# Performance work log

Measured on AMD Instinct MI355X. Metric: run time of the kernel, lower is better.

The kernel has to match this reference:

```python
import jax, jax.numpy as jnp
import numpy as np

HIDDEN = 768  # hidden_dim of the embedding matrix
VOCAB = 30522


def setup_inputs() -> dict:
    key = jax.random.key(0)
    k1, k2, k3, k4, k5, k6 = jax.random.split(key, 6)
    core = jax.random.normal(k1, (40, 256, 256), dtype=jnp.float32)
    f0 = jax.random.normal(k2, (40, 40), dtype=jnp.float32)
    f1 = jax.random.normal(k3, (768, 256), dtype=jnp.float32)
    f2 = jax.random.normal(k4, (768, 256), dtype=jnp.float32)
    ids = jax.random.randint(k5, (8192,), 0, VOCAB, dtype=jnp.int32)
    x = jax.random.normal(k6, (8192, 768), dtype=jnp.float32)  # unused by forward, kept for signature parity
    return {"x": x, "ids": ids, "core": core, "f0": f0, "f1": f1, "f2": f2}


def reference(x, ids, core, f0, f1, f2):
    # tucker_to_tensor: core x_0 f0 x_1 f1 x_2 f2 -> (40, 768, 768)
    res = jnp.einsum('abc,ia,jb,kc->ijk', core, f0, f1, f2)
    # flatten to padded embedding table (30720, 768) and gather requested rows
    table = res.reshape(-1, HIDDEN)
    return table[ids, :]
```

## Files before the change

kernel.cpp:

```cpp
#include <hip/hip_runtime.h>


#define A_DIM 40
#define BC 65536
#define C_DIM 256
#define HID 768

typedef __attribute__((ext_vector_type(8))) short short8;
typedef __attribute__((ext_vector_type(4))) float floatx4;

#define AS1 __attribute__((address_space(1)))
#define AS3 __attribute__((address_space(3)))

__device__ __forceinline__ void gl2lds16(const unsigned short* g, unsigned short* l) {
    __builtin_amdgcn_global_load_lds((const AS1 unsigned int*)g, (AS3 unsigned int*)l,
                                     16, 0, 0);
}

__device__ __forceinline__ unsigned short f2bf(float f) {
    unsigned int u = __builtin_bit_cast(unsigned int, f);
    u += 0x7FFFu + ((u >> 16) & 1u);
    return (unsigned short)(u >> 16);
}

__global__ __launch_bounds__(256) void k01_fused(const float* __restrict__ core,
                                                 const float* __restrict__ f0,
                                                 const float* __restrict__ f1,
                                                 const float* __restrict__ f2,
                                                 unsigned short* __restrict__ A1t,
                                                 unsigned short* __restrict__ f1b,
                                                 unsigned short* __restrict__ f2b) {
    const int bid = blockIdx.x;
    const int tid = threadIdx.x;
    if (bid < 512) {
        __shared__ float f0s[200];
        __shared__ unsigned short tt[32 * 34];
        const int i0 = (bid >> 6) * 5;
        const int tile = bid & 63;
        const int b0 = (tile >> 3) * 32;
        const int c0 = (tile & 7) * 32;
        if (tid < 200) f0s[tid] = f0[i0 * A_DIM + tid];
        __syncthreads();

        const int pb = (tid >> 4) * 2;
        const int pc = (tid & 15) * 2;
        float acc[5][4];
#pragma unroll
        for (int ii = 0; ii < 5; ++ii)
#pragma unroll
            for (int e = 0; e < 4; ++e) acc[ii][e] = 0.f;

        const float* cp0 = core + (b0 + pb) * 256 + (c0 + pc);
        for (int a = 0; a < A_DIM; ++a) {
            const float* cp = cp0 + a * BC;
            const float2 r0 = *(const float2*)cp;
            const float2 r1 = *(const float2*)(cp + 256);
#pragma unroll
            for (int ii = 0; ii < 5; ++ii) {
                const float fa = f0s[ii * A_DIM + a];
                acc[ii][0] += fa * r0.x;
                acc[ii][1] += fa * r0.y;
                acc[ii][2] += fa * r1.x;
                acc[ii][3] += fa * r1.y;
            }
        }
        const int rc = tid >> 3;
        const int rb4 = (tid & 7) * 4;
#pragma unroll
        for (int ii = 0; ii < 5; ++ii) {
            if (ii) __syncthreads();
            unsigned short e00 = f2bf(acc[ii][0]);
            unsigned short e10 = f2bf(acc[ii][2]);
            unsigned short e01 = f2bf(acc[ii][1]);
            unsigned short e11 = f2bf(acc[ii][3]);
            *(unsigned int*)&tt[pc * 34 + pb]       = (unsigned int)e00 | ((unsigned int)e10 << 16);
            *(unsigned int*)&tt[(pc + 1) * 34 + pb] = (unsigned int)e01 | ((unsigned int)e11 << 16);
            __syncthreads();
            unsigned short o[4];
#pragma unroll
            for (int u = 0; u < 4; ++u) o[u] = tt[rc * 34 + rb4 + u];
            unsigned int lo = (unsigned int)o[0] | ((unsigned int)o[1] << 16);
            unsigned int hi = (unsigned int)o[2] | ((unsigned int)o[3] << 16);
            *(uint2*)&A1t[(size_t)(i0 + ii) * BC + (c0 + rc) * 256 + b0 + rb4] = make_uint2(lo, hi);
        }
    } else {
        const int idx = (bid - 512) * 256 + tid;
        const float* src;
        unsigned short* dst;
        int off;
        if (idx < 49152) { src = f1; dst = f1b; off = idx; }
        else             { src = f2; dst = f2b; off = idx - 49152; }
        const float4 v = *(const float4*)&src[off * 4];
        const unsigned int lo = (unsigned int)f2bf(v.x) | ((unsigned int)f2bf(v.y) << 16);
        const unsigned int hi = (unsigned int)f2bf(v.z) | ((unsigned int)f2bf(v.w) << 16);
        *(uint2*)&dst[off * 4] = make_uint2(lo, hi);
    }
}

__global__ __launch_bounds__(256) void k2_gemm(const unsigned short* __restrict__ f1b,
                                               const unsigned short* __restrict__ A1t,
                                               unsigned short* __restrict__ A2) {
    const int i  = blockIdx.z;
    const int j0 = blockIdx.x * 64;
    const int c0 = blockIdx.y * 64;
    const unsigned short* __restrict__ Bsrc = A1t + i * BC;

    __shared__ unsigned short As[64 * 32];
    __shared__ unsigned short Bs[64 * 32];

    const int tid = threadIdx.x;
    const int lane = tid & 63, wave = tid >> 6;
    const int wm = (wave >> 1) * 32, wn = (wave & 1) * 32;
    const int l16 = lane & 15, q = lane >> 4;

    const int r0 = tid >> 2, o0 = (tid & 3) * 8;
    unsigned short* AsW = &As[wave * 512];
    unsigned short* BsW = &Bs[wave * 512];

    floatx4 acc[2][2];
#pragma unroll
    for (int p = 0; p < 2; ++p)
#pragma unroll
        for (int r = 0; r < 2; ++r) acc[p][r] = (floatx4)0.f;

    for (int kk = 0; kk < C_DIM; kk += 32) {
        gl2lds16(&f1b[(j0 + r0) * 256 + kk + o0], AsW);
        gl2lds16(&Bsrc[(c0 + r0) * 256 + kk + o0], BsW);
        __syncthreads();
        short8 af[2], bf[2];
#pragma unroll
        for (int p = 0; p < 2; ++p) af[p] = *(const short8*)&As[(wm + p * 16 + l16) * 32 + q * 8];
#pragma unroll
        for (int r = 0; r < 2; ++r) bf[r] = *(const short8*)&Bs[(wn + r * 16 + l16) * 32 + q * 8];
#pragma unroll
        for (int p = 0; p < 2; ++p)
#pragma unroll
            for (int r = 0; r < 2; ++r)
                acc[p][r] = __builtin_amdgcn_mfma_f32_16x16x32_bf16(af[p], bf[r], acc[p][r], 0, 0, 0);
        __syncthreads();
    }
    unsigned short* __restrict__ Cout = A2 + (size_t)i * HID * C_DIM;
#pragma unroll
    for (int p = 0; p < 2; ++p)
#pragma unroll
        for (int r = 0; r < 2; ++r)
#pragma unroll
            for (int rr = 0; rr < 4; ++rr) {
                const int row = j0 + wm + p * 16 + q * 4 + rr;
                const int col = c0 + wn + r * 16 + l16;
                Cout[row * 256 + col] = f2bf(acc[p][r][rr]);
            }
}

__global__ __launch_bounds__(256) void k3_gemm(const unsigned short* __restrict__ A2,
                                               const unsigned short* __restrict__ f2b,
                                               const int* __restrict__ ids,
                                               float* __restrict__ out) {
    const int n0 = blockIdx.x * 64;
    const int k0 = blockIdx.y * 64;

    __shared__ int ids_s[64];
    __shared__ unsigned short As[64 * 32];
    __shared__ unsigned short Bs[64 * 32];

    const int tid = threadIdx.x;
    if (tid < 64) ids_s[tid] = ids[n0 + tid];
    __syncthreads();

    const int lane = tid & 63, wave = tid >> 6;
    const int wm = (wave >> 1) * 32, wn = (wave & 1) * 32;
    const int l16 = lane & 15, q = lane >> 4;

    const int r0 = tid >> 2, o0 = (tid & 3) * 8;
    const size_t ga = (size_t)ids_s[r0] * 256;
    unsigned short* AsW = &As[wave * 512];
    unsigned short* BsW = &Bs[wave * 512];

    floatx4 acc[2][2];
#pragma unroll
    for (int p = 0; p < 2; ++p)
#pragma unroll
        for (int r = 0; r < 2; ++r) acc[p][r] = (floatx4)0.f;

    for (int kk = 0; kk < C_DIM; kk += 32) {
        gl2lds16(&A2[ga + kk + o0], AsW);
        gl2lds16(&f2b[(k0 + r0) * 256 + kk + o0], BsW);
        __syncthreads();
        short8 af[2], bf[2];
#pragma unroll
        for (int p = 0; p < 2; ++p) af[p] = *(const short8*)&As[(wm + p * 16 + l16) * 32 + q * 8];
#pragma unroll
        for (int r = 0; r < 2; ++r) bf[r] = *(const short8*)&Bs[(wn + r * 16 + l16) * 32 + q * 8];
#pragma unroll
        for (int p = 0; p < 2; ++p)
#pragma unroll
            for (int r = 0; r < 2; ++r)
                acc[p][r] = __builtin_amdgcn_mfma_f32_16x16x32_bf16(af[p], bf[r], acc[p][r], 0, 0, 0);
        __syncthreads();
    }
#pragma unroll
    for (int p = 0; p < 2; ++p)
#pragma unroll
        for (int r = 0; r < 2; ++r)
#pragma unroll
            for (int rr = 0; rr < 4; ++rr) {
                const int row = n0 + wm + p * 16 + q * 4 + rr;
                const int col = k0 + wn + r * 16 + l16;
                out[(size_t)row * HID + col] = acc[p][r][rr];
            }
}

extern "C" void kernel_launch(void* const* d_in, const int* in_sizes, int n_in,
                              void* d_out, int out_size, void* d_ws, size_t ws_size,
                              hipStream_t stream) {
    const int*   ids  = (const int*)d_in[1];
    const float* core = (const float*)d_in[2];
    const float* f0   = (const float*)d_in[3];
    const float* f1   = (const float*)d_in[4];
    const float* f2   = (const float*)d_in[5];
    float* out = (float*)d_out;

    char* ws = (char*)d_ws;
    unsigned short* A1t = (unsigned short*)ws;
    unsigned short* A2  = (unsigned short*)(ws + 5242880);
    unsigned short* f1b = (unsigned short*)(ws + 20971520);
    unsigned short* f2b = (unsigned short*)(ws + 21364736);

    k01_fused<<<896, 256, 0, stream>>>(core, f0, f1, f2, A1t, f1b, f2b);
    k2_gemm<<<dim3(12, 4, A_DIM), 256, 0, stream>>>(f1b, A1t, A2);
    k3_gemm<<<dim3(128, 12), 256, 0, stream>>>(A2, f2b, ids, out);
}
```

Before: 113.5 us.

## Compute only the intermediate rows that the ids gather actually needs

An extra block in the first kernel buckets the ids by their leading index i, records the requested j rows per i in slot lists padded to 64, and stores a tile count per i. The second GEMM now runs one block per tile of requested rows, gathering f1 rows through the slot list, instead of computing all 768 rows for every i. This cuts the second GEMM's work to roughly the rows the final gather touches. In exchange it adds a serial, atomic-heavy bucketing block, and it assumes at most 320 ids fall on any one i (CAP). Inputs that concentrate more ids on a single i would overflow the slot buffer.

Measured after the change: 121.3 us. +6.9%, slower.

```diff
diff --git a/kernel.cpp b/kernel.cpp
--- a/kernel.cpp
+++ b/kernel.cpp
@@ -5,6 +5,7 @@
 #define BC 65536
 #define C_DIM 256
 #define HID 768
+#define CAP 320
 
 typedef __attribute__((ext_vector_type(8))) short short8;
 typedef __attribute__((ext_vector_type(4))) float floatx4;
@@ -27,9 +28,12 @@
                                                  const float* __restrict__ f0,
                                                  const float* __restrict__ f1,
                                                  const float* __restrict__ f2,
+                                                 const int* __restrict__ ids,
                                                  unsigned short* __restrict__ A1t,
                                                  unsigned short* __restrict__ f1b,
-                                                 unsigned short* __restrict__ f2b) {
+                                                 unsigned short* __restrict__ f2b,
+                                                 int* __restrict__ jslot,
+                                                 int* __restrict__ tilecnt) {
     const int bid = blockIdx.x;
     const int tid = threadIdx.x;
     if (bid < 512) {
@@ -83,7 +87,7 @@
             unsigned int hi = (unsigned int)o[2] | ((unsigned int)o[3] << 16);
             *(uint2*)&A1t[(size_t)(i0 + ii) * BC + (c0 + rc) * 256 + b0 + rb4] = make_uint2(lo, hi);
         }
-    } else {
+    } else if (bid < 896) {
         const int idx = (bid - 512) * 256 + tid;
         const float* src;
         unsigned short* dst;
@@ -94,26 +98,58 @@
         const unsigned int lo = (unsigned int)f2bf(v.x) | ((unsigned int)f2bf(v.y) << 16);
         const unsigned int hi = (unsigned int)f2bf(v.z) | ((unsigned int)f2bf(v.w) << 16);
         *(uint2*)&dst[off * 4] = make_uint2(lo, hi);
+    } else {
+        __shared__ int cnt[A_DIM];
+        __shared__ int off[A_DIM];
+        if (tid < A_DIM) { cnt[tid] = 0; off[tid] = 0; }
+        __syncthreads();
+        for (int t = tid; t < 8192; t += 256) {
+            const unsigned int id = (unsigned int)ids[t];
+            atomicAdd(&cnt[id / 768], 1);
+        }
+        __syncthreads();
+        for (int t = tid; t < 8192; t += 256) {
+            const unsigned int id = (unsigned int)ids[t];
+            const int i = id / 768;
+            const int s = atomicAdd(&off[i], 1);
+            jslot[i * CAP + s] = (int)(id - i * 768u);
+        }
+        __syncthreads();
+        if (tid < A_DIM) {
+            const int u = cnt[tid];
+            const int tc = (u + 63) >> 6;
+            tilecnt[tid] = tc;
+            for (int s = u; s < tc * 64; ++s) jslot[tid * CAP + s] = 0;
+        }
     }
 }
 
 __global__ __launch_bounds__(256) void k2_gemm(const unsigned short* __restrict__ f1b,
                                                const unsigned short* __restrict__ A1t,
+                                               const int* __restrict__ jslot,
+                                               const int* __restrict__ tilecnt,
                                                unsigned short* __restrict__ A2) {
-    const int i  = blockIdx.z;
-    const int j0 = blockIdx.x * 64;
-    const int c0 = blockIdx.y * 64;
+    const int T = blockIdx.y;
+    const int i = T / 5, t = T % 5;
+    if (t >= tilecnt[i]) return;
+    const int c0 = blockIdx.x * 64;
+    const int slot0 = i * CAP + t * 64;
     const unsigned short* __restrict__ Bsrc = A1t + i * BC;
 
+    __shared__ int js[64];
     __shared__ unsigned short As[64 * 32];
     __shared__ unsigned short Bs[64 * 32];
 
     const int tid = threadIdx.x;
+    if (tid < 64) js[tid] = jslot[slot0 + tid];
+    __syncthreads();
+
     const int lane = tid & 63, wave = tid >> 6;
     const int wm = (wave >> 1) * 32, wn = (wave & 1) * 32;
     const int l16 = lane & 15, q = lane >> 4;
 
     const int r0 = tid >> 2, o0 = (tid & 3) * 8;
+    const size_t ga = (size_t)js[r0] * 256;
     unsigned short* AsW = &As[wave * 512];
     unsigned short* BsW = &Bs[wave * 512];
 
@@ -124,7 +160,7 @@
         for (int r = 0; r < 2; ++r) acc[p][r] = (floatx4)0.f;
 
     for (int kk = 0; kk < C_DIM; kk += 32) {
-        gl2lds16(&f1b[(j0 + r0) * 256 + kk + o0], AsW);
+        gl2lds16(&f1b[ga + kk + o0], AsW);
         gl2lds16(&Bsrc[(c0 + r0) * 256 + kk + o0], BsW);
         __syncthreads();
         short8 af[2], bf[2];
@@ -139,16 +175,15 @@
                 acc[p][r] = __builtin_amdgcn_mfma_f32_16x16x32_bf16(af[p], bf[r], acc[p][r], 0, 0, 0);
         __syncthreads();
     }
-    unsigned short* __restrict__ Cout = A2 + (size_t)i * HID * C_DIM;
 #pragma unroll
     for (int p = 0; p < 2; ++p)
 #pragma unroll
         for (int r = 0; r < 2; ++r)
 #pragma unroll
             for (int rr = 0; rr < 4; ++rr) {
-                const int row = j0 + wm + p * 16 + q * 4 + rr;
+                const int jrow = js[wm + p * 16 + q * 4 + rr];
                 const int col = c0 + wn + r * 16 + l16;
-                Cout[row * 256 + col] = f2bf(acc[p][r][rr]);
+                A2[(size_t)(i * HID + jrow) * 256 + col] = f2bf(acc[p][r][rr]);
             }
 }
 
@@ -221,12 +256,14 @@
     float* out = (float*)d_out;
 
     char* ws = (char*)d_ws;
-    unsigned short* A1t = (unsigned short*)ws;
-    unsigned short* A2  = (unsigned short*)(ws + 5242880);
-    unsigned short* f1b = (unsigned short*)(ws + 20971520);
-    unsigned short* f2b = (unsigned short*)(ws + 21364736);
-
-    k01_fused<<<896, 256, 0, stream>>>(core, f0, f1, f2, A1t, f1b, f2b);
-    k2_gemm<<<dim3(12, 4, A_DIM), 256, 0, stream>>>(f1b, A1t, A2);
+    unsigned short* A1t   = (unsigned short*)ws;
+    unsigned short* A2    = (unsigned short*)(ws + 5242880);
+    unsigned short* f1b   = (unsigned short*)(ws + 20971520);
+    unsigned short* f2b   = (unsigned short*)(ws + 21364736);
+    int*            jslot = (int*)(ws + 21757952);
+    int*            tcnt  = (int*)(ws + 21809152);
+
+    k01_fused<<<897, 256, 0, stream>>>(core, f0, f1, f2, ids, A1t, f1b, f2b, jslot, tcnt);
+    k2_gemm<<<dim3(4, 200), 256, 0, stream>>>(f1b, A1t, jslot, tcnt, A2);
     k3_gemm<<<dim3(128, 12), 256, 0, stream>>>(A2, f2b, ids, out);
 }
```
